# Performance work log

Hardware: AMD Instinct MI355X
Metric: run time of the kernel (lower is better)

Reference implementation:

```python
import jax, jax.numpy as jnp
import numpy as np

K = 1  # number of items to sample exactly
B, N = 512, 8192


def log1mexp(x):
    # log(1 - exp(x)) for x <= 0, numerically stable (Maechler 2012)
    return jnp.where(x > -jnp.log(2.0), jnp.log(-jnp.expm1(x)), jnp.log1p(-jnp.exp(x)))


def logaddexp_c(x1, x2):
    # custom logaddexp matching the torch module (handles -inf == -inf ties)
    delta = jnp.where(x1 == x2, 0.0, x1 - x2)
    return jnp.maximum(x1, x2) + jax.nn.softplus(-jnp.abs(delta))


def dp_table(logp, logq, kk):
    # a[b, i, c] = log Pr(exactly c-1 successes among first i items); shape [B, n+1, kk+2]
    bsz = logp.shape[0]
    state0 = jnp.full((bsz, kk + 2), -jnp.inf, logp.dtype).at[:, 1].set(0.0)
    ninf_col = jnp.full((bsz, 1), -jnp.inf, logp.dtype)

    def step(state, xs):
        lp, lq = xs  # each [B]
        grown = logaddexp_c(state[:, :-1] + lp[:, None], state[:, 1:] + lq[:, None])
        new = jnp.concatenate([ninf_col, grown], axis=1)
        return new, new

    _, rows = jax.lax.scan(step, state0, (logp.T, logq.T))  # rows: [n, B, kk+2]
    return jnp.concatenate([state0[None], rows], axis=0).transpose(1, 0, 2)


def sample_scan(a, logp, noise):
    # reverse DP sampling pass; a: [B, n+1, C], logp/noise: [B, n]
    bsz, np1, C = a.shape
    n = np1 - 1
    kcol = C - 1  # == K + 1 in table-column coordinates
    ap = a[:, :-1, :][:, ::-1].transpose(1, 0, 2)  # [n, B, C], row i-1 for i=n..1
    ac = a[:, 1:, :][:, ::-1].transpose(1, 0, 2)   # [n, B, C], row i   for i=n..1
    lp_rev = logp[:, ::-1].T                        # [n, B]
    u_rev = noise[:, ::-1].T                        # [n, B]

    def step(j, xs):
        ap_r, ac_r, lp_t, u_t = xs
        p = jnp.take_along_axis(ap_r, (j - 1)[:, None], axis=1)[:, 0]
        z = jnp.take_along_axis(ac_r, j[:, None], axis=1)[:, 0]
        p = jnp.minimum(p + lp_t - z, 0.0)  # conditional log-prob, clamp fp round-off
        q = log1mexp(p)
        X = (u_t < jax.nn.sigmoid(p - q)).astype(logp.dtype)  # Bernoulli(logits=p-q)
        j = jnp.where(X > 0, j - 1, j)
        return j, X

    j0 = jnp.full((bsz,), kcol, jnp.int32)
    _, Xs = jax.lax.scan(step, j0, (ap, ac, lp_rev, u_rev))  # Xs: [n, B]
    return Xs[::-1].T  # [B, n]


def setup_inputs() -> dict:
    key = jax.random.key(0)
    k1, k2 = jax.random.split(key)
    logits = jax.random.normal(k1, (B, N), dtype=jnp.float32)
    noise = jax.random.uniform(k2, (B, N), dtype=jnp.float32)
    return {"logits": logits, "noise": noise}


def reference(logits, noise):
    logp = jnp.minimum(jax.nn.log_sigmoid(logits), -1e-7)  # clamped log_sigmoid
    logq = log1mexp(logp)
    a = dp_table(logp, logq, K)       # [B, N+1, K+2]
    return sample_scan(a, logp, noise)  # [B, N] in {0,1}
```

## Files before the change

### kernel.cpp

```cpp
#include <hip/hip_runtime.h>
#include <math.h>
#include <stdint.h>

#define NB 512
#define NI 8192
#define NG (NI / 4)
#define NLOG2 0.69314718055994530942f

__device__ __forceinline__ float log1mexp_f(float x) {
    return (x > -NLOG2) ? logf(-expm1f(x)) : log1pf(-expf(x));
}

__device__ float g_P[(size_t)NB * NI];

#define TB 64
#define TK 16
__global__ __launch_bounds__(256) void prep_kernel(const float* __restrict__ logits,
                                                   float* __restrict__ Alp,
                                                   float* __restrict__ Blq) {
    __shared__ float4 lp_t[TB][TK + 1];
    __shared__ float4 lq_t[TB][TK + 1];
    int bx = blockIdx.x;
    int tb = (bx & 7) * TB;
    int tkb = (bx >> 3) * TK;
    int t = threadIdx.x;

    int kl = t & 15;
    int rl0 = t >> 4;
#pragma unroll
    for (int r = 0; r < 4; ++r) {
        int row_local = r * 16 + rl0;
        float4 x4 = *(const float4*)&logits[(size_t)(tb + row_local) * NI + (size_t)(tkb + kl) * 4];
        float4 lp4, lq4;
        const float* xs = &x4.x;
        float* lps = &lp4.x;
        float* lqs = &lq4.x;
#pragma unroll
        for (int j = 0; j < 4; ++j) {
            float x = xs[j];
            float lp = -(fmaxf(-x, 0.0f) + log1pf(expf(-fabsf(x))));
            lp = fminf(lp, -1e-7f);
            lps[j] = lp;
            lqs[j] = log1mexp_f(lp);
        }
        lp_t[row_local][kl] = lp4;
        lq_t[row_local][kl] = lq4;
    }
    __syncthreads();

    int bl = t & 63;
    int kw0 = t >> 6;
#pragma unroll
    for (int w = 0; w < 4; ++w) {
        int k_local = w * 4 + kw0;
        size_t dst = (size_t)(tkb + k_local) * NB + (size_t)(tb + bl);
        ((float4*)Alp)[dst] = lp_t[bl][k_local];
        ((float4*)Blq)[dst] = lq_t[bl][k_local];
    }
}

__device__ __forceinline__ void scan_step_p(float lp, float lq, float& S0, float& S1,
                                            float& po) {
    const float L2E = 1.44269504088896340736f;
    const float LN2 = 0.69314718055994530942f;
    float x1 = S0 + lp;
    float x2 = S1 + lq;
    float d  = x1 - x2;
    float m  = fmaxf(x1, x2);
    float z  = fabsf(d) * -L2E;
    float e  = __builtin_amdgcn_exp2f(z);
    float a  = 1.0f + e;
    float l  = __builtin_amdgcn_logf(a);
    S1 = fmaf(l, LN2, m);
    S0 = S0 + lq;
    po = fminf(x1 - S1, 0.0f);
}

#define CH 8
#define SB() __builtin_amdgcn_sched_barrier(0)

__global__ __launch_bounds__(64, 1) void scan_kernel(const float* __restrict__ A,
                                                     const float* __restrict__ B) {
    int row = blockIdx.x * 64 + threadIdx.x;
    const float4* Ap = (const float4*)A;
    const float4* Bp = (const float4*)B;
    float4* Pp = (float4*)g_P;

    float S0 = 0.0f, S1 = -INFINITY;
    float4 lpE[CH], lqE[CH], lpO[CH], lqO[CH];

#pragma unroll
    for (int j = 0; j < CH; ++j) {
        lpE[j] = Ap[(size_t)j * NB + row];
        lqE[j] = Bp[(size_t)j * NB + row];
    }
#pragma unroll
    for (int j = 0; j < CH; ++j) {
        lpO[j] = Ap[(size_t)(CH + j) * NB + row];
        lqO[j] = Bp[(size_t)(CH + j) * NB + row];
    }

    const int NCHUNK = NG / CH;
    for (int c = 0; c < NCHUNK; c += 2) {
        SB();
#pragma unroll
        for (int j = 0; j < CH; ++j) {
            float4 p4;
            scan_step_p(lpE[j].x, lqE[j].x, S0, S1, p4.x);
            scan_step_p(lpE[j].y, lqE[j].y, S0, S1, p4.y);
            scan_step_p(lpE[j].z, lqE[j].z, S0, S1, p4.z);
            scan_step_p(lpE[j].w, lqE[j].w, S0, S1, p4.w);
            Pp[(size_t)(c * CH + j) * NB + row] = p4;
        }
        SB();
        {
            int g2 = ((c + 2) & (NCHUNK - 1)) * CH;
#pragma unroll
            for (int j = 0; j < CH; ++j) {
                lpE[j] = Ap[(size_t)(g2 + j) * NB + row];
                lqE[j] = Bp[(size_t)(g2 + j) * NB + row];
            }
        }
        SB();
#pragma unroll
        for (int j = 0; j < CH; ++j) {
            float4 p4;
            scan_step_p(lpO[j].x, lqO[j].x, S0, S1, p4.x);
            scan_step_p(lpO[j].y, lqO[j].y, S0, S1, p4.y);
            scan_step_p(lpO[j].z, lqO[j].z, S0, S1, p4.z);
            scan_step_p(lpO[j].w, lqO[j].w, S0, S1, p4.w);
            Pp[(size_t)((c + 1) * CH + j) * NB + row] = p4;
        }
        SB();
        {
            int g3 = ((c + 3) & (NCHUNK - 1)) * CH;
#pragma unroll
            for (int j = 0; j < CH; ++j) {
                lpO[j] = Ap[(size_t)(g3 + j) * NB + row];
                lqO[j] = Bp[(size_t)(g3 + j) * NB + row];
            }
        }
    }
}

__global__ __launch_bounds__(256) void decide_kernel(const float* __restrict__ noise,
                                                     float* __restrict__ out) {
    int row = blockIdx.x;
    const float4* pp = (const float4*)g_P;
    const float4* ur = (const float4*)(noise + (size_t)row * NI);
    float4* outr = (float4*)(out + (size_t)row * NI);
    int tid = threadIdx.x;

    int best = -1;
#pragma unroll
    for (int k = 0; k < NG / 256; ++k) {
        int g = tid + k * 256;
        float4 p4 = pp[(size_t)g * NB + row];
        float4 u = ur[g];
#pragma unroll
        for (int j = 0; j < 4; ++j) {
            float p = (&p4.x)[j];
            float q = log1mexp_f(p);
            float z = p - q;
            float prob = 1.0f / (1.0f + expf(-z));
            if ((&u.x)[j] < prob) {
                int i = 4 * g + j;
                best = (i > best) ? i : best;
            }
        }
    }

#pragma unroll
    for (int off = 32; off > 0; off >>= 1) {
        int o = __shfl_down(best, off);
        best = (o > best) ? o : best;
    }
    __shared__ int lds[4];
    __shared__ int sel_s;
    int wid = tid >> 6;
    if ((tid & 63) == 0) lds[wid] = best;
    __syncthreads();
    if (tid == 0) {
        int s01 = (lds[0] > lds[1]) ? lds[0] : lds[1];
        int s23 = (lds[2] > lds[3]) ? lds[2] : lds[3];
        sel_s = (s01 > s23) ? s01 : s23;
    }
    __syncthreads();
    int sel = sel_s;

#pragma unroll
    for (int k = 0; k < NG / 256; ++k) {
        int g = tid + k * 256;
        int i0 = 4 * g;
        float4 v;
        v.x = (i0 == sel) ? 1.0f : 0.0f;
        v.y = (i0 + 1 == sel) ? 1.0f : 0.0f;
        v.z = (i0 + 2 == sel) ? 1.0f : 0.0f;
        v.w = (i0 + 3 == sel) ? 1.0f : 0.0f;
        outr[g] = v;
    }
}

extern "C" void kernel_launch(void* const* d_in, const int* in_sizes, int n_in,
                              void* d_out, int out_size, void* d_ws, size_t ws_size,
                              hipStream_t stream) {
    (void)in_sizes; (void)n_in; (void)out_size; (void)ws_size;
    const float* logits = (const float*)d_in[0];
    const float* noise = (const float*)d_in[1];
    float* out = (float*)d_out;
    float* A = (float*)d_ws;

    prep_kernel<<<8 * (NG / TK), 256, 0, stream>>>(logits, A, out);
    scan_kernel<<<8, 64, 0, stream>>>(A, out);
    decide_kernel<<<NB, 256, 0, stream>>>(noise, out);
}
```

Measured before the change: 420.6 us.

## Rotate scan chunks across four wavefronts to hide load latency

The sequential scan kernel now uses four wavefronts per block, taking turns round-robin on consecutive chunks. The scan state is handed between them through shared memory, and each wave prefetches its next chunk while the others compute. This replaces the single-wave double buffering with explicit sched barriers, so memory latency is hidden by other waves instead of one wave's register buffers. The cost is a block-wide barrier per chunk plus shared-memory state traffic on the serial critical path.

```diff
diff --git a/kernel.cpp b/kernel.cpp
--- a/kernel.cpp
+++ b/kernel.cpp
@@ -76,70 +76,55 @@
     po = fminf(x1 - S1, 0.0f);
 }
 
-#define CH 8
-#define SB() __builtin_amdgcn_sched_barrier(0)
-
-__global__ __launch_bounds__(64, 1) void scan_kernel(const float* __restrict__ A,
-                                                     const float* __restrict__ B) {
-    int row = blockIdx.x * 64 + threadIdx.x;
+#define CHR 8
+#define WV 4
+
+__global__ __launch_bounds__(256, 1) void scan_kernel(const float* __restrict__ A,
+                                                      const float* __restrict__ B) {
+    int lane = threadIdx.x & 63;
+    int w = threadIdx.x >> 6;
+    int row = blockIdx.x * 64 + lane;
     const float4* Ap = (const float4*)A;
     const float4* Bp = (const float4*)B;
     float4* Pp = (float4*)g_P;
 
-    float S0 = 0.0f, S1 = -INFINITY;
-    float4 lpE[CH], lqE[CH], lpO[CH], lqO[CH];
-
-#pragma unroll
-    for (int j = 0; j < CH; ++j) {
-        lpE[j] = Ap[(size_t)j * NB + row];
-        lqE[j] = Bp[(size_t)j * NB + row];
-    }
-#pragma unroll
-    for (int j = 0; j < CH; ++j) {
-        lpO[j] = Ap[(size_t)(CH + j) * NB + row];
-        lqO[j] = Bp[(size_t)(CH + j) * NB + row];
-    }
-
-    const int NCHUNK = NG / CH;
-    for (int c = 0; c < NCHUNK; c += 2) {
-        SB();
-#pragma unroll
-        for (int j = 0; j < CH; ++j) {
-            float4 p4;
-            scan_step_p(lpE[j].x, lqE[j].x, S0, S1, p4.x);
-            scan_step_p(lpE[j].y, lqE[j].y, S0, S1, p4.y);
-            scan_step_p(lpE[j].z, lqE[j].z, S0, S1, p4.z);
-            scan_step_p(lpE[j].w, lqE[j].w, S0, S1, p4.w);
-            Pp[(size_t)(c * CH + j) * NB + row] = p4;
-        }
-        SB();
-        {
-            int g2 = ((c + 2) & (NCHUNK - 1)) * CH;
-#pragma unroll
-            for (int j = 0; j < CH; ++j) {
-                lpE[j] = Ap[(size_t)(g2 + j) * NB + row];
-                lqE[j] = Bp[(size_t)(g2 + j) * NB + row];
+    __shared__ float S0s[64], S1s[64];
+    if (threadIdx.x < 64) { S0s[threadIdx.x] = 0.0f; S1s[threadIdx.x] = -INFINITY; }
+
+    float4 lpR[CHR], lqR[CHR];
+#pragma unroll
+    for (int j = 0; j < CHR; ++j) {
+        lpR[j] = Ap[(size_t)(w * CHR + j) * NB + row];
+        lqR[j] = Bp[(size_t)(w * CHR + j) * NB + row];
+    }
+    __syncthreads();
+
+    const int NCHUNK = NG / CHR;
+    for (int c = 0; c < NCHUNK; ++c) {
+        if ((c & (WV - 1)) == w) {
+            float S0 = S0s[lane];
+            float S1 = S1s[lane];
+#pragma unroll
+            for (int j = 0; j < CHR; ++j) {
+                float4 p4;
+                scan_step_p(lpR[j].x, lqR[j].x, S0, S1, p4.x);
+                scan_step_p(lpR[j].y, lqR[j].y, S0, S1, p4.y);
+                scan_step_p(lpR[j].z, lqR[j].z, S0, S1, p4.z);
+                scan_step_p(lpR[j].w, lqR[j].w, S0, S1, p4.w);
+                Pp[(size_t)(c * CHR + j) * NB + row] = p4;
+            }
+            S0s[lane] = S0;
+            S1s[lane] = S1;
+            int cn = c + WV;
+            if (cn < NCHUNK) {
+#pragma unroll
+                for (int j = 0; j < CHR; ++j) {
+                    lpR[j] = Ap[(size_t)(cn * CHR + j) * NB + row];
+                    lqR[j] = Bp[(size_t)(cn * CHR + j) * NB + row];
+                }
             }
         }
-        SB();
-#pragma unroll
-        for (int j = 0; j < CH; ++j) {
-            float4 p4;
-            scan_step_p(lpO[j].x, lqO[j].x, S0, S1, p4.x);
-            scan_step_p(lpO[j].y, lqO[j].y, S0, S1, p4.y);
-            scan_step_p(lpO[j].z, lqO[j].z, S0, S1, p4.z);
-            scan_step_p(lpO[j].w, lqO[j].w, S0, S1, p4.w);
-            Pp[(size_t)((c + 1) * CH + j) * NB + row] = p4;
-        }
-        SB();
-        {
-            int g3 = ((c + 3) & (NCHUNK - 1)) * CH;
-#pragma unroll
-            for (int j = 0; j < CH; ++j) {
-                lpO[j] = Ap[(size_t)(g3 + j) * NB + row];
-                lqO[j] = Bp[(size_t)(g3 + j) * NB + row];
-            }
-        }
+        __syncthreads();
     }
 }
 
@@ -211,6 +196,6 @@
     float* A = (float*)d_ws;
 
     prep_kernel<<<8 * (NG / TK), 256, 0, stream>>>(logits, A, out);
-    scan_kernel<<<8, 64, 0, stream>>>(A, out);
+    scan_kernel<<<8, 256, 0, stream>>>(A, out);
     decide_kernel<<<NB, 256, 0, stream>>>(noise, out);
 }
```

Result: no change. 418.3 us (-0.5%).
